# Optimization experiments

Measured on AMD Instinct MI355X. Metric: run time of the kernel, lower is better.

## Reference

```python
import jax, jax.numpy as jnp
import numpy as np

T, H, I, E, TOPK = 1024, 1024, 2048, 8, 2


def setup_inputs() -> dict:
    key = jax.random.key(0)
    k1, k2, k3, k4, k5, k6 = jax.random.split(key, 6)
    hidden_states = jax.random.normal(k1, (T, H), dtype=jnp.float32)
    expert_affinities = jax.random.uniform(k2, (T, E), dtype=jnp.float32)
    expert_index = jax.random.randint(k3, (T, TOPK), 0, E, dtype=jnp.int64)
    # Expert GLU MLP weights: gate/up [E,H,I], down [E,I,H]
    w_gate = jax.random.normal(k4, (E, H, I), dtype=jnp.float32) / np.sqrt(H)
    w_up = jax.random.normal(k5, (E, H, I), dtype=jnp.float32) / np.sqrt(H)
    w_down = jax.random.normal(k6, (E, I, H), dtype=jnp.float32) / np.sqrt(I)
    return {
        "hidden_states": hidden_states,
        "expert_affinities": expert_affinities,
        "expert_index": expert_index,
        "w_gate": w_gate,
        "w_up": w_up,
        "w_down": w_down,
        "seq_len": T,
    }


def reference(hidden_states, expert_affinities, expert_index, w_gate, w_up, w_down, seq_len):
    # Gather top-k affinities and renormalize (normalize_top_k_affinities=True)
    topk_aff = jnp.take_along_axis(expert_affinities, expert_index, axis=1)  # [T,K]
    topk_aff = topk_aff / jnp.sum(topk_aff, axis=1, keepdims=True)
    # Dense combine weights [T,E] (scatter of normalized top-k affinities)
    t_idx = jnp.arange(hidden_states.shape[0])[:, None]
    combine = jnp.zeros((hidden_states.shape[0], w_gate.shape[0]),
                        dtype=hidden_states.dtype).at[t_idx, expert_index].add(topk_aff)
    # GLU expert MLP for all experts (E small, grouped-GEMM form)
    g = jnp.einsum("th,ehi->tei", hidden_states, w_gate)  # [T,E,I]
    u = jnp.einsum("th,ehi->tei", hidden_states, w_up)    # [T,E,I]
    act = jax.nn.silu(g) * u                               # [T,E,I]
    # Down-projection fused with affinity-weighted combine
    out = jnp.einsum("tei,eih,te->th", act, w_down, combine)  # [T,H]
    return out
```

## Files before the change

kernel.cpp:

```cpp
#include <hip/hip_runtime.h>
#include <hip/hip_bf16.h>
#include <math.h>

#define T_ 1024
#define H_ 1024
#define I_ 2048
#define E_ 8
#define NSLOT 2048

#define BM 128
#define BN 64
#define BK 32
#define CHUNKS_PER_E (NSLOT / BM)
#define SPLITK2 2

typedef __attribute__((ext_vector_type(8))) short bf16x8;
typedef __attribute__((ext_vector_type(4))) float f32x4;
typedef __attribute__((ext_vector_type(4))) unsigned uint4v;

#define MFMA_BF16 __builtin_amdgcn_mfma_f32_16x16x32_bf16

__device__ __forceinline__ short f2bf(float f) {
  union { float f; unsigned u; } v; v.f = f;
  unsigned r = v.u + 0x7FFFu + ((v.u >> 16) & 1u);
  return (short)(r >> 16);
}
__device__ __forceinline__ unsigned cvtpk(float lo, float hi) {
  unsigned r;
  asm("v_cvt_pk_bf16_f32 %0, %1, %2" : "=v"(r) : "v"(lo), "v"(hi));
  return r;
}
__device__ __forceinline__ void gll16(const void* g, void* l) {
  __builtin_amdgcn_global_load_lds(
      (const __attribute__((address_space(1))) void*)g,
      (__attribute__((address_space(3))) void*)l, 16, 0, 0);
}

__device__ __forceinline__ void pipe_barrier() {
  __builtin_amdgcn_sched_barrier(0);
  asm volatile("s_waitcnt vmcnt(3) lgkmcnt(0)" ::: "memory");
  __builtin_amdgcn_s_barrier();
  __builtin_amdgcn_sched_barrier(0);
}
__device__ __forceinline__ void drain_barrier() {
  __builtin_amdgcn_sched_barrier(0);
  asm volatile("s_waitcnt vmcnt(0) lgkmcnt(0)" ::: "memory");
  __builtin_amdgcn_s_barrier();
  __builtin_amdgcn_sched_barrier(0);
}

__device__ __forceinline__ unsigned bswz(int n, int kbyte) {
  return (unsigned)(n * 64 + (kbyte ^ (((n >> 2) & 3) << 4)));
}

__global__ __launch_bounds__(256) void k_prep(const float* __restrict__ hs,
                                              short* __restrict__ hs_bf) {
  int i = (blockIdx.x * 256 + threadIdx.x) * 8;
  float4 v0 = *(const float4*)&hs[i];
  float4 v1 = *(const float4*)&hs[i + 4];
  uint4v p;
  p.x = cvtpk(v0.x, v0.y); p.y = cvtpk(v0.z, v0.w);
  p.z = cvtpk(v1.x, v1.y); p.w = cvtpk(v1.z, v1.w);
  *(uint4v*)&hs_bf[i] = p;
}

__global__ __launch_bounds__(1024) void k_build(
    const float* __restrict__ aff, const int* __restrict__ eidx,
    int* __restrict__ offs, int* __restrict__ slot_tok, float* __restrict__ slot_w) {
  __shared__ int cnt[E_];
  __shared__ int soff[E_ + 1];
  int t = threadIdx.x;
  if (t < E_) cnt[t] = 0;
  __syncthreads();
  int e0 = eidx[t * 2 + 0];
  int e1 = eidx[t * 2 + 1];
  float a0 = aff[t * E_ + e0];
  float a1 = aff[t * E_ + e1];
  float inv = 1.0f / (a0 + a1);
  int r0 = atomicAdd(&cnt[e0], 1);
  int r1 = atomicAdd(&cnt[e1], 1);
  __syncthreads();
  if (t == 0) {
    int s = 0;
    for (int e = 0; e < E_; ++e) { soff[e] = s; s += cnt[e]; }
    soff[E_] = s;
  }
  __syncthreads();
  if (t <= E_) offs[t] = soff[t];
  int s0 = soff[e0] + r0;
  int s1 = soff[e1] + r1;
  slot_tok[s0] = t; slot_w[s0] = a0 * inv;
  slot_tok[s1] = t; slot_w[s1] = a1 * inv;
}

__global__ __launch_bounds__(512, 4) void k_gemm1(
    const short* __restrict__ hs_bf, const float* __restrict__ wg,
    const float* __restrict__ wu, const int* __restrict__ offs,
    const int* __restrict__ slot_tok, short* __restrict__ act) {
  int e = blockIdx.y >> 4;
  int chunk = blockIdx.y & (CHUNKS_PER_E - 1);
  int lo = offs[e], hi = offs[e + 1];
  int row0 = lo + chunk * BM;
  if (row0 >= hi) return;
  int rows = min(BM, hi - row0);
  int i0 = blockIdx.x * BN;

  __shared__ short sA[4][BM * BK];
  __shared__ short sB[2][2][BN * BK];

  int tid = threadIdx.x;
  int lane = tid & 63;
  int w = tid >> 6;
  int wm = w >> 1, wn = w & 1;
  int lr = lane & 15;
  int lk = (lane >> 4) * 8;

  const float* wgE = wg + (size_t)e * H_ * I_;
  const float* wuE = wu + (size_t)e * H_ * I_;

  int ra = 16 * w + (lane >> 2);
  int tokA = slot_tok[row0 + min(ra, rows - 1)];
  const short* srcA = hs_bf + (size_t)tokA * H_ + (lane & 3) * 8;
  const float* wB = (w < 4) ? wgE : wuE;
  int mat = (w >= 4);
  int up = 4 * (w & 3) + (lane >> 4);
  int n4 = (lane & 15) * 4;
  const float* srcB = wB + (size_t)(2 * up) * I_ + i0 + n4;

  f32x4 accg[2][2], accu[2][2];
#pragma unroll
  for (int mr = 0; mr < 2; ++mr)
#pragma unroll
    for (int nr = 0; nr < 2; ++nr) {
      accg[mr][nr] = (f32x4){0.f, 0.f, 0.f, 0.f};
      accu[mr][nr] = (f32x4){0.f, 0.f, 0.f, 0.f};
    }

  float4 bs[2][2];

  gll16(srcA, &sA[0][w * 512]);
  bs[0][0] = *(const float4*)srcB;
  bs[0][1] = *(const float4*)(srcB + I_);
  gll16(srcA + BK, &sA[1][w * 512]);
  bs[1][0] = *(const float4*)(srcB + (size_t)BK * I_);
  bs[1][1] = *(const float4*)(srcB + (size_t)(BK + 1) * I_);
  {
    const float* p0 = (const float*)&bs[0][0];
    const float* p1 = (const float*)&bs[0][1];
#pragma unroll
    for (int j = 0; j < 4; ++j)
      *(unsigned*)((char*)&sB[0][mat][0] + bswz(n4 + j, 4 * up)) = cvtpk(p0[j], p1[j]);
  }
  drain_barrier();

  const int NT = H_ / BK;

#define G1_ITER(U, base_) do {                                                 \
    int t_ = (base_) + (U);                                                    \
    if (t_ + 2 < NT) {                                                         \
      int k2 = (t_ + 2) * BK;                                                  \
      gll16(srcA + k2, &sA[((U) + 2) & 3][w * 512]);                           \
      bs[(U) & 1][0] = *(const float4*)(srcB + (size_t)k2 * I_);               \
      bs[(U) & 1][1] = *(const float4*)(srcB + (size_t)(k2 + 1) * I_);         \
    }                                                                          \
    bf16x8 a0 = *(const bf16x8*)&sA[(U)][(wm * 32 + lr) * BK + lk];            \
    bf16x8 a1 = *(const bf16x8*)&sA[(U)][(wm * 32 + 16 + lr) * BK + lk];       \
    unsigned off0 = bswz(wn * 32 + lr, lk * 2);                                \
    unsigned off1 = bswz(wn * 32 + 16 + lr, lk * 2);                           \
    bf16x8 bg0 = *(const bf16x8*)((const char*)&sB[(U) & 1][0][0] + off0);     \
    bf16x8 bg1 = *(const bf16x8*)((const char*)&sB[(U) & 1][0][0] + off1);     \
    bf16x8 bu0 = *(const bf16x8*)((const char*)&sB[(U) & 1][1][0] + off0);     \
    bf16x8 bu1 = *(const bf16x8*)((const char*)&sB[(U) & 1][1][0] + off1);     \
    accg[0][0] = MFMA_BF16(a0, bg0, accg[0][0], 0, 0, 0);                      \
    accg[0][1] = MFMA_BF16(a0, bg1, accg[0][1], 0, 0, 0);                      \
    accg[1][0] = MFMA_BF16(a1, bg0, accg[1][0], 0, 0, 0);                      \
    accg[1][1] = MFMA_BF16(a1, bg1, accg[1][1], 0, 0, 0);                      \
    accu[0][0] = MFMA_BF16(a0, bu0, accu[0][0], 0, 0, 0);                      \
    accu[0][1] = MFMA_BF16(a0, bu1, accu[0][1], 0, 0, 0);                      \
    accu[1][0] = MFMA_BF16(a1, bu0, accu[1][0], 0, 0, 0);                      \
    accu[1][1] = MFMA_BF16(a1, bu1, accu[1][1], 0, 0, 0);                      \
    if (t_ + 1 < NT) {                                                         \
      const float* p0 = (const float*)&bs[((U) + 1) & 1][0];                   \
      const float* p1 = (const float*)&bs[((U) + 1) & 1][1];                   \
      _Pragma("unroll")                                                        \
      for (int j = 0; j < 4; ++j)                                              \
        *(unsigned*)((char*)&sB[((U) + 1) & 1][mat][0] + bswz(n4 + j, 4 * up)) \
            = cvtpk(p0[j], p1[j]);                                             \
    }                                                                          \
    pipe_barrier();                                                            \
  } while (0)

  for (int base = 0; base < NT; base += 4) {
    G1_ITER(0, base);
    G1_ITER(1, base);
    G1_ITER(2, base);
    G1_ITER(3, base);
  }
#undef G1_ITER

#pragma unroll
  for (int mr = 0; mr < 2; ++mr) {
#pragma unroll
    for (int r = 0; r < 4; ++r) {
      int m = wm * 32 + mr * 16 + (lane >> 4) * 4 + r;
      if (m < rows) {
#pragma unroll
        for (int nr = 0; nr < 2; ++nr) {
          float g = accg[mr][nr][r];
          float u = accu[mr][nr][r];
          float sg = 1.0f / (1.0f + __expf(-g));
          act[(size_t)(row0 + m) * I_ + i0 + wn * 32 + nr * 16 + lr] = f2bf(g * sg * u);
        }
      }
    }
  }
}

__global__ __launch_bounds__(512, 4) void k_gemm2(
    const short* __restrict__ act, const float* __restrict__ wd,
    const int* __restrict__ offs, const int* __restrict__ slot_tok,
    const float* __restrict__ slot_w, float* __restrict__ out) {
  int e = blockIdx.y >> 4;
  int chunk = blockIdx.y & (CHUNKS_PER_E - 1);
  int lo = offs[e], hi = offs[e + 1];
  int row0 = lo + chunk * BM;
  if (row0 >= hi) return;
  int rows = min(BM, hi - row0);
  int h0 = blockIdx.x * BN;
  int kbase = blockIdx.z * (I_ / SPLITK2);

  __shared__ short sA[4][BM * BK];
  __shared__ short sB[2][BN * BK];

  int tid = threadIdx.x;
  int lane = tid & 63;
  int w = tid >> 6;
  int wm = w >> 1, wn = w & 1;
  int lr = lane & 15;
  int lk = (lane >> 4) * 8;

  const float* wdE = wd + (size_t)e * I_ * H_;

  int ra = min(16 * w + (lane >> 2), rows - 1);
  const short* srcA = act + (size_t)(row0 + ra) * I_ + kbase + (lane & 3) * 8;
  int up = tid >> 5;
  int n2 = (tid & 31) * 2;
  const float* srcB = wdE + (size_t)(kbase + 2 * up) * H_ + h0 + n2;

  f32x4 acc[2][2];
#pragma unroll
  for (int mr = 0; mr < 2; ++mr)
#pragma unroll
    for (int nr = 0; nr < 2; ++nr)
      acc[mr][nr] = (f32x4){0.f, 0.f, 0.f, 0.f};

  float2 bs[2][2];

  gll16(srcA, &sA[0][w * 512]);
  bs[0][0] = *(const float2*)srcB;
  bs[0][1] = *(const float2*)(srcB + H_);
  gll16(srcA + BK, &sA[1][w * 512]);
  bs[1][0] = *(const float2*)(srcB + (size_t)BK * H_);
  bs[1][1] = *(const float2*)(srcB + (size_t)(BK + 1) * H_);
  *(unsigned*)((char*)&sB[0][0] + bswz(n2, 4 * up))     = cvtpk(bs[0][0].x, bs[0][1].x);
  *(unsigned*)((char*)&sB[0][0] + bswz(n2 + 1, 4 * up)) = cvtpk(bs[0][0].y, bs[0][1].y);
  drain_barrier();

  const int NT = (I_ / SPLITK2) / BK;

#define G2_ITER(U, base_) do {                                                 \
    int t_ = (base_) + (U);                                                    \
    if (t_ + 2 < NT) {                                                         \
      int k2 = (t_ + 2) * BK;                                                  \
      gll16(srcA + k2, &sA[((U) + 2) & 3][w * 512]);                           \
      bs[(U) & 1][0] = *(const float2*)(srcB + (size_t)k2 * H_);               \
      bs[(U) & 1][1] = *(const float2*)(srcB + (size_t)(k2 + 1) * H_);         \
    }                                                                          \
    bf16x8 a0 = *(const bf16x8*)&sA[(U)][(wm * 32 + lr) * BK + lk];            \
    bf16x8 a1 = *(const bf16x8*)&sA[(U)][(wm * 32 + 16 + lr) * BK + lk];       \
    bf16x8 b0 = *(const bf16x8*)((const char*)&sB[(U) & 1][0]                  \
                                 + bswz(wn * 32 + lr, lk * 2));                \
    bf16x8 b1 = *(const bf16x8*)((const char*)&sB[(U) & 1][0]                  \
                                 + bswz(wn * 32 + 16 + lr, lk * 2));           \
    acc[0][0] = MFMA_BF16(a0, b0, acc[0][0], 0, 0, 0);                         \
    acc[0][1] = MFMA_BF16(a0, b1, acc[0][1], 0, 0, 0);                         \
    acc[1][0] = MFMA_BF16(a1, b0, acc[1][0], 0, 0, 0);                         \
    acc[1][1] = MFMA_BF16(a1, b1, acc[1][1], 0, 0, 0);                         \
    if (t_ + 1 < NT) {                                                         \
      *(unsigned*)((char*)&sB[((U) + 1) & 1][0] + bswz(n2, 4 * up))            \
          = cvtpk(bs[((U) + 1) & 1][0].x, bs[((U) + 1) & 1][1].x);             \
      *(unsigned*)((char*)&sB[((U) + 1) & 1][0] + bswz(n2 + 1, 4 * up))        \
          = cvtpk(bs[((U) + 1) & 1][0].y, bs[((U) + 1) & 1][1].y);             \
    }                                                                          \
    pipe_barrier();                                                            \
  } while (0)

  for (int base = 0; base < NT; base += 4) {
    G2_ITER(0, base);
    G2_ITER(1, base);
    G2_ITER(2, base);
    G2_ITER(3, base);
  }
#undef G2_ITER

#pragma unroll
  for (int mr = 0; mr < 2; ++mr) {
#pragma unroll
    for (int r = 0; r < 4; ++r) {
      int m = wm * 32 + mr * 16 + (lane >> 4) * 4 + r;
      if (m < rows) {
        int gs = row0 + m;
        float wc = slot_w[gs];
        int tok = slot_tok[gs];
#pragma unroll
        for (int nr = 0; nr < 2; ++nr)
          atomicAdd(&out[(size_t)tok * H_ + h0 + wn * 32 + nr * 16 + lr],
                    acc[mr][nr][r] * wc);
      }
    }
  }
}

extern "C" void kernel_launch(void* const* d_in, const int* in_sizes, int n_in,
                              void* d_out, int out_size, void* d_ws, size_t ws_size,
                              hipStream_t stream) {
  const float* hs   = (const float*)d_in[0];
  const float* aff  = (const float*)d_in[1];
  const int*   eidx = (const int*)d_in[2];
  const float* wg   = (const float*)d_in[3];
  const float* wu   = (const float*)d_in[4];
  const float* wd   = (const float*)d_in[5];
  float* out = (float*)d_out;

  char* ws = (char*)d_ws;
  int*   offs     = (int*)ws;
  int*   slot_tok = (int*)(ws + 64);
  float* slot_w   = (float*)(ws + 64 + NSLOT * 4);
  short* hs_bf    = (short*)(ws + 64 + NSLOT * 8);
  short* act      = (short*)(ws + 64 + NSLOT * 8 + (size_t)T_ * H_ * 2);

  hipMemsetAsync(d_out, 0, (size_t)out_size * sizeof(float), stream);
  k_build<<<1, T_, 0, stream>>>(aff, eidx, offs, slot_tok, slot_w);
  k_prep<<<(T_ * H_) / (256 * 8), 256, 0, stream>>>(hs, hs_bf);
  k_gemm1<<<dim3(I_ / BN, E_ * CHUNKS_PER_E), 512, 0, stream>>>(hs_bf, wg, wu, offs, slot_tok, act);
  k_gemm2<<<dim3(H_ / BN, E_ * CHUNKS_PER_E, SPLITK2), 512, 0, stream>>>(act, wd, offs, slot_tok, slot_w, out);
}
```

Measured before the change: 105.5 us.

## Compact chunk list, narrow N tile, 4-wave blocks with swizzled A tiles

The routing kernel now emits a compact list of (expert, row-start) chunks, so both GEMM grids cover only real chunks (cap 24) instead of launching 16 mostly-empty chunk slots per expert. The N tile shrinks from 64 to 32 and blocks drop from 8 to 4 waves, each covering 32 rows with two A loads per step. An XOR swizzle is added to the A shared-memory tile to cut bank conflicts, and the wait counts are adjusted for the extra in-flight loads. This removes idle blocks and adds more blocks along N, at the cost of re-reading the A tile more often per output column. A NCHUNK_CAP of 24 assumes per-expert counts stay small enough; larger imbalance would silently drop chunks.

```diff
diff --git a/kernel.cpp b/kernel.cpp
--- a/kernel.cpp
+++ b/kernel.cpp
@@ -9,9 +9,9 @@
 #define NSLOT 2048
 
 #define BM 128
-#define BN 64
+#define BN 32
 #define BK 32
-#define CHUNKS_PER_E (NSLOT / BM)
+#define NCHUNK_CAP 24
 #define SPLITK2 2
 
 typedef __attribute__((ext_vector_type(8))) short bf16x8;
@@ -36,9 +36,15 @@
       (__attribute__((address_space(3))) void*)l, 16, 0, 0);
 }
 
-__device__ __forceinline__ void pipe_barrier() {
-  __builtin_amdgcn_sched_barrier(0);
-  asm volatile("s_waitcnt vmcnt(3) lgkmcnt(0)" ::: "memory");
+__device__ __forceinline__ void pipe_barrier6() {
+  __builtin_amdgcn_sched_barrier(0);
+  asm volatile("s_waitcnt vmcnt(6) lgkmcnt(0)" ::: "memory");
+  __builtin_amdgcn_s_barrier();
+  __builtin_amdgcn_sched_barrier(0);
+}
+__device__ __forceinline__ void pipe_barrier4() {
+  __builtin_amdgcn_sched_barrier(0);
+  asm volatile("s_waitcnt vmcnt(4) lgkmcnt(0)" ::: "memory");
   __builtin_amdgcn_s_barrier();
   __builtin_amdgcn_sched_barrier(0);
 }
@@ -51,6 +57,9 @@
 
 __device__ __forceinline__ unsigned bswz(int n, int kbyte) {
   return (unsigned)(n * 64 + (kbyte ^ (((n >> 2) & 3) << 4)));
+}
+__device__ __forceinline__ unsigned aswz(int r, int kbyte) {
+  return (unsigned)(r * 64 + (kbyte ^ (((r >> 1) & 3) << 4)));
 }
 
 __global__ __launch_bounds__(256) void k_prep(const float* __restrict__ hs,
@@ -66,7 +75,7 @@
 
 __global__ __launch_bounds__(1024) void k_build(
     const float* __restrict__ aff, const int* __restrict__ eidx,
-    int* __restrict__ offs, int* __restrict__ slot_tok, float* __restrict__ slot_w) {
+    int* __restrict__ meta, int* __restrict__ slot_tok, float* __restrict__ slot_w) {
   __shared__ int cnt[E_];
   __shared__ int soff[E_ + 1];
   int t = threadIdx.x;
@@ -84,25 +93,31 @@
     int s = 0;
     for (int e = 0; e < E_; ++e) { soff[e] = s; s += cnt[e]; }
     soff[E_] = s;
+    int nc = 0;
+    for (int e = 0; e < E_; ++e)
+      for (int c = soff[e]; c < soff[e] + cnt[e]; c += BM)
+        meta[16 + nc++] = e | (c << 8);
+    meta[9] = nc;
   }
   __syncthreads();
-  if (t <= E_) offs[t] = soff[t];
+  if (t <= E_) meta[t] = soff[t];
   int s0 = soff[e0] + r0;
   int s1 = soff[e1] + r1;
   slot_tok[s0] = t; slot_w[s0] = a0 * inv;
   slot_tok[s1] = t; slot_w[s1] = a1 * inv;
 }
 
-__global__ __launch_bounds__(512, 4) void k_gemm1(
+__global__ __launch_bounds__(256, 4) void k_gemm1(
     const short* __restrict__ hs_bf, const float* __restrict__ wg,
-    const float* __restrict__ wu, const int* __restrict__ offs,
+    const float* __restrict__ wu, const int* __restrict__ meta,
     const int* __restrict__ slot_tok, short* __restrict__ act) {
-  int e = blockIdx.y >> 4;
-  int chunk = blockIdx.y & (CHUNKS_PER_E - 1);
-  int lo = offs[e], hi = offs[e + 1];
-  int row0 = lo + chunk * BM;
-  if (row0 >= hi) return;
-  int rows = min(BM, hi - row0);
+  int nch = meta[9];
+  int yc = blockIdx.y;
+  if (yc >= nch) return;
+  int ck = meta[16 + yc];
+  int e = ck & 255;
+  int row0 = ck >> 8;
+  int rows = min(BM, meta[1 + e] - row0);
   int i0 = blockIdx.x * BN;
 
   __shared__ short sA[4][BM * BK];
@@ -111,21 +126,24 @@
   int tid = threadIdx.x;
   int lane = tid & 63;
   int w = tid >> 6;
-  int wm = w >> 1, wn = w & 1;
   int lr = lane & 15;
-  int lk = (lane >> 4) * 8;
+  int q = lane >> 4;
+  int lk = q * 8;
 
   const float* wgE = wg + (size_t)e * H_ * I_;
   const float* wuE = wu + (size_t)e * H_ * I_;
 
-  int ra = 16 * w + (lane >> 2);
-  int tokA = slot_tok[row0 + min(ra, rows - 1)];
-  const short* srcA = hs_bf + (size_t)tokA * H_ + (lane & 3) * 8;
-  const float* wB = (w < 4) ? wgE : wuE;
-  int mat = (w >= 4);
-  int up = 4 * (w & 3) + (lane >> 4);
-  int n4 = (lane & 15) * 4;
-  const float* srcB = wB + (size_t)(2 * up) * I_ + i0 + n4;
+  int r1 = 32 * w + (lane >> 2);
+  int kgel = ((lane & 3) ^ ((lane >> 3) & 3)) * 8;
+  int tok1 = slot_tok[row0 + min(r1, rows - 1)];
+  int tok2 = slot_tok[row0 + min(r1 + 16, rows - 1)];
+  const short* srcA1 = hs_bf + (size_t)tok1 * H_ + kgel;
+  const short* srcA2 = hs_bf + (size_t)tok2 * H_ + kgel;
+
+  int up = tid >> 4;
+  int n2 = (tid & 15) * 2;
+  const float* srcBg = wgE + (size_t)(2 * up) * I_ + i0 + n2;
+  const float* srcBu = wuE + (size_t)(2 * up) * I_ + i0 + n2;
 
   f32x4 accg[2][2], accu[2][2];
 #pragma unroll
@@ -136,21 +154,24 @@
       accu[mr][nr] = (f32x4){0.f, 0.f, 0.f, 0.f};
     }
 
-  float4 bs[2][2];
-
-  gll16(srcA, &sA[0][w * 512]);
-  bs[0][0] = *(const float4*)srcB;
-  bs[0][1] = *(const float4*)(srcB + I_);
-  gll16(srcA + BK, &sA[1][w * 512]);
-  bs[1][0] = *(const float4*)(srcB + (size_t)BK * I_);
-  bs[1][1] = *(const float4*)(srcB + (size_t)(BK + 1) * I_);
-  {
-    const float* p0 = (const float*)&bs[0][0];
-    const float* p1 = (const float*)&bs[0][1];
-#pragma unroll
-    for (int j = 0; j < 4; ++j)
-      *(unsigned*)((char*)&sB[0][mat][0] + bswz(n4 + j, 4 * up)) = cvtpk(p0[j], p1[j]);
-  }
+  float2 bg[2][2], bu[2][2];
+
+  gll16(srcA1, &sA[0][w * 1024]);
+  gll16(srcA2, &sA[0][w * 1024 + 512]);
+  bg[0][0] = *(const float2*)srcBg;
+  bg[0][1] = *(const float2*)(srcBg + I_);
+  bu[0][0] = *(const float2*)srcBu;
+  bu[0][1] = *(const float2*)(srcBu + I_);
+  gll16(srcA1 + BK, &sA[1][w * 1024]);
+  gll16(srcA2 + BK, &sA[1][w * 1024 + 512]);
+  bg[1][0] = *(const float2*)(srcBg + (size_t)BK * I_);
+  bg[1][1] = *(const float2*)(srcBg + (size_t)(BK + 1) * I_);
+  bu[1][0] = *(const float2*)(srcBu + (size_t)BK * I_);
+  bu[1][1] = *(const float2*)(srcBu + (size_t)(BK + 1) * I_);
+  *(unsigned*)((char*)&sB[0][0][0] + bswz(n2, 4 * up))     = cvtpk(bg[0][0].x, bg[0][1].x);
+  *(unsigned*)((char*)&sB[0][0][0] + bswz(n2 + 1, 4 * up)) = cvtpk(bg[0][0].y, bg[0][1].y);
+  *(unsigned*)((char*)&sB[0][1][0] + bswz(n2, 4 * up))     = cvtpk(bu[0][0].x, bu[0][1].x);
+  *(unsigned*)((char*)&sB[0][1][0] + bswz(n2 + 1, 4 * up)) = cvtpk(bu[0][0].y, bu[0][1].y);
   drain_barrier();
 
   const int NT = H_ / BK;
@@ -159,35 +180,43 @@
     int t_ = (base_) + (U);                                                    \
     if (t_ + 2 < NT) {                                                         \
       int k2 = (t_ + 2) * BK;                                                  \
-      gll16(srcA + k2, &sA[((U) + 2) & 3][w * 512]);                           \
-      bs[(U) & 1][0] = *(const float4*)(srcB + (size_t)k2 * I_);               \
-      bs[(U) & 1][1] = *(const float4*)(srcB + (size_t)(k2 + 1) * I_);         \
+      gll16(srcA1 + k2, &sA[((U) + 2) & 3][w * 1024]);                         \
+      gll16(srcA2 + k2, &sA[((U) + 2) & 3][w * 1024 + 512]);                   \
+      bg[(U) & 1][0] = *(const float2*)(srcBg + (size_t)k2 * I_);              \
+      bg[(U) & 1][1] = *(const float2*)(srcBg + (size_t)(k2 + 1) * I_);        \
+      bu[(U) & 1][0] = *(const float2*)(srcBu + (size_t)k2 * I_);              \
+      bu[(U) & 1][1] = *(const float2*)(srcBu + (size_t)(k2 + 1) * I_);        \
     }                                                                          \
-    bf16x8 a0 = *(const bf16x8*)&sA[(U)][(wm * 32 + lr) * BK + lk];            \
-    bf16x8 a1 = *(const bf16x8*)&sA[(U)][(wm * 32 + 16 + lr) * BK + lk];       \
-    unsigned off0 = bswz(wn * 32 + lr, lk * 2);                                \
-    unsigned off1 = bswz(wn * 32 + 16 + lr, lk * 2);                           \
-    bf16x8 bg0 = *(const bf16x8*)((const char*)&sB[(U) & 1][0][0] + off0);     \
-    bf16x8 bg1 = *(const bf16x8*)((const char*)&sB[(U) & 1][0][0] + off1);     \
-    bf16x8 bu0 = *(const bf16x8*)((const char*)&sB[(U) & 1][1][0] + off0);     \
-    bf16x8 bu1 = *(const bf16x8*)((const char*)&sB[(U) & 1][1][0] + off1);     \
-    accg[0][0] = MFMA_BF16(a0, bg0, accg[0][0], 0, 0, 0);                      \
-    accg[0][1] = MFMA_BF16(a0, bg1, accg[0][1], 0, 0, 0);                      \
-    accg[1][0] = MFMA_BF16(a1, bg0, accg[1][0], 0, 0, 0);                      \
-    accg[1][1] = MFMA_BF16(a1, bg1, accg[1][1], 0, 0, 0);                      \
-    accu[0][0] = MFMA_BF16(a0, bu0, accu[0][0], 0, 0, 0);                      \
-    accu[0][1] = MFMA_BF16(a0, bu1, accu[0][1], 0, 0, 0);                      \
-    accu[1][0] = MFMA_BF16(a1, bu0, accu[1][0], 0, 0, 0);                      \
-    accu[1][1] = MFMA_BF16(a1, bu1, accu[1][1], 0, 0, 0);                      \
+    bf16x8 a0 = *(const bf16x8*)((const char*)&sA[(U)][0]                      \
+                                 + aswz(w * 32 + lr, lk * 2));                 \
+    bf16x8 a1 = *(const bf16x8*)((const char*)&sA[(U)][0]                      \
+                                 + aswz(w * 32 + 16 + lr, lk * 2));            \
+    unsigned off0 = bswz(lr, lk * 2);                                          \
+    unsigned off1 = bswz(16 + lr, lk * 2);                                     \
+    bf16x8 fg0 = *(const bf16x8*)((const char*)&sB[(U) & 1][0][0] + off0);     \
+    bf16x8 fg1 = *(const bf16x8*)((const char*)&sB[(U) & 1][0][0] + off1);     \
+    bf16x8 fu0 = *(const bf16x8*)((const char*)&sB[(U) & 1][1][0] + off0);     \
+    bf16x8 fu1 = *(const bf16x8*)((const char*)&sB[(U) & 1][1][0] + off1);     \
+    accg[0][0] = MFMA_BF16(a0, fg0, accg[0][0], 0, 0, 0);                      \
+    accg[0][1] = MFMA_BF16(a0, fg1, accg[0][1], 0, 0, 0);                      \
+    accg[1][0] = MFMA_BF16(a1, fg0, accg[1][0], 0, 0, 0);                      \
+    accg[1][1] = MFMA_BF16(a1, fg1, accg[1][1], 0, 0, 0);                      \
+    accu[0][0] = MFMA_BF16(a0, fu0, accu[0][0], 0, 0, 0);                      \
+    accu[0][1] = MFMA_BF16(a0, fu1, accu[0][1], 0, 0, 0);                      \
+    accu[1][0] = MFMA_BF16(a1, fu0, accu[1][0], 0, 0, 0);                      \
+    accu[1][1] = MFMA_BF16(a1, fu1, accu[1][1], 0, 0, 0);                      \
     if (t_ + 1 < NT) {                                                         \
-      const float* p0 = (const float*)&bs[((U) + 1) & 1][0];                   \
-      const float* p1 = (const float*)&bs[((U) + 1) & 1][1];                   \
-      _Pragma("unroll")                                                        \
-      for (int j = 0; j < 4; ++j)                                              \
-        *(unsigned*)((char*)&sB[((U) + 1) & 1][mat][0] + bswz(n4 + j, 4 * up)) \
-            = cvtpk(p0[j], p1[j]);                                             \
+      int s_ = ((U) + 1) & 1;                                                  \
+      *(unsigned*)((char*)&sB[s_][0][0] + bswz(n2, 4 * up))                    \
+          = cvtpk(bg[s_][0].x, bg[s_][1].x);                                   \
+      *(unsigned*)((char*)&sB[s_][0][0] + bswz(n2 + 1, 4 * up))                \
+          = cvtpk(bg[s_][0].y, bg[s_][1].y);                                   \
+      *(unsigned*)((char*)&sB[s_][1][0] + bswz(n2, 4 * up))                    \
+          = cvtpk(bu[s_][0].x, bu[s_][1].x);                                   \
+      *(unsigned*)((char*)&sB[s_][1][0] + bswz(n2 + 1, 4 * up))                \
+          = cvtpk(bu[s_][0].y, bu[s_][1].y);                                   \
     }                                                                          \
-    pipe_barrier();                                                            \
+    pipe_barrier6();                                                           \
   } while (0)
 
   for (int base = 0; base < NT; base += 4) {
@@ -202,30 +231,31 @@
   for (int mr = 0; mr < 2; ++mr) {
 #pragma unroll
     for (int r = 0; r < 4; ++r) {
-      int m = wm * 32 + mr * 16 + (lane >> 4) * 4 + r;
+      int m = w * 32 + mr * 16 + q * 4 + r;
       if (m < rows) {
 #pragma unroll
         for (int nr = 0; nr < 2; ++nr) {
           float g = accg[mr][nr][r];
           float u = accu[mr][nr][r];
           float sg = 1.0f / (1.0f + __expf(-g));
-          act[(size_t)(row0 + m) * I_ + i0 + wn * 32 + nr * 16 + lr] = f2bf(g * sg * u);
+          act[(size_t)(row0 + m) * I_ + i0 + nr * 16 + lr] = f2bf(g * sg * u);
         }
       }
     }
   }
 }
 
-__global__ __launch_bounds__(512, 4) void k_gemm2(
+__global__ __launch_bounds__(256, 4) void k_gemm2(
     const short* __restrict__ act, const float* __restrict__ wd,
-    const int* __restrict__ offs, const int* __restrict__ slot_tok,
+    const int* __restrict__ meta, const int* __restrict__ slot_tok,
     const float* __restrict__ slot_w, float* __restrict__ out) {
-  int e = blockIdx.y >> 4;
-  int chunk = blockIdx.y & (CHUNKS_PER_E - 1);
-  int lo = offs[e], hi = offs[e + 1];
-  int row0 = lo + chunk * BM;
-  if (row0 >= hi) return;
-  int rows = min(BM, hi - row0);
+  int nch = meta[9];
+  int yc = blockIdx.y;
+  if (yc >= nch) return;
+  int ck = meta[16 + yc];
+  int e = ck & 255;
+  int row0 = ck >> 8;
+  int rows = min(BM, meta[1 + e] - row0);
   int h0 = blockIdx.x * BN;
   int kbase = blockIdx.z * (I_ / SPLITK2);
 
@@ -235,16 +265,19 @@
   int tid = threadIdx.x;
   int lane = tid & 63;
   int w = tid >> 6;
-  int wm = w >> 1, wn = w & 1;
   int lr = lane & 15;
-  int lk = (lane >> 4) * 8;
+  int q = lane >> 4;
+  int lk = q * 8;
 
   const float* wdE = wd + (size_t)e * I_ * H_;
 
-  int ra = min(16 * w + (lane >> 2), rows - 1);
-  const short* srcA = act + (size_t)(row0 + ra) * I_ + kbase + (lane & 3) * 8;
-  int up = tid >> 5;
-  int n2 = (tid & 31) * 2;
+  int r1 = 32 * w + (lane >> 2);
+  int kgel = ((lane & 3) ^ ((lane >> 3) & 3)) * 8;
+  const short* srcA1 = act + (size_t)(row0 + min(r1, rows - 1)) * I_ + kbase + kgel;
+  const short* srcA2 = act + (size_t)(row0 + min(r1 + 16, rows - 1)) * I_ + kbase + kgel;
+
+  int up = tid >> 4;
+  int n2 = (tid & 15) * 2;
   const float* srcB = wdE + (size_t)(kbase + 2 * up) * H_ + h0 + n2;
 
   f32x4 acc[2][2];
@@ -254,16 +287,18 @@
     for (int nr = 0; nr < 2; ++nr)
       acc[mr][nr] = (f32x4){0.f, 0.f, 0.f, 0.f};
 
-  float2 bs[2][2];
-
-  gll16(srcA, &sA[0][w * 512]);
-  bs[0][0] = *(const float2*)srcB;
-  bs[0][1] = *(const float2*)(srcB + H_);
-  gll16(srcA + BK, &sA[1][w * 512]);
-  bs[1][0] = *(const float2*)(srcB + (size_t)BK * H_);
-  bs[1][1] = *(const float2*)(srcB + (size_t)(BK + 1) * H_);
-  *(unsigned*)((char*)&sB[0][0] + bswz(n2, 4 * up))     = cvtpk(bs[0][0].x, bs[0][1].x);
-  *(unsigned*)((char*)&sB[0][0] + bswz(n2 + 1, 4 * up)) = cvtpk(bs[0][0].y, bs[0][1].y);
+  float2 bd[2][2];
+
+  gll16(srcA1, &sA[0][w * 1024]);
+  gll16(srcA2, &sA[0][w * 1024 + 512]);
+  bd[0][0] = *(const float2*)srcB;
+  bd[0][1] = *(const float2*)(srcB + H_);
+  gll16(srcA1 + BK, &sA[1][w * 1024]);
+  gll16(srcA2 + BK, &sA[1][w * 1024 + 512]);
+  bd[1][0] = *(const float2*)(srcB + (size_t)BK * H_);
+  bd[1][1] = *(const float2*)(srcB + (size_t)(BK + 1) * H_);
+  *(unsigned*)((char*)&sB[0][0] + bswz(n2, 4 * up))     = cvtpk(bd[0][0].x, bd[0][1].x);
+  *(unsigned*)((char*)&sB[0][0] + bswz(n2 + 1, 4 * up)) = cvtpk(bd[0][0].y, bd[0][1].y);
   drain_barrier();
 
   const int NT = (I_ / SPLITK2) / BK;
@@ -272,27 +307,31 @@
     int t_ = (base_) + (U);                                                    \
     if (t_ + 2 < NT) {                                                         \
       int k2 = (t_ + 2) * BK;                                                  \
-      gll16(srcA + k2, &sA[((U) + 2) & 3][w * 512]);                           \
-      bs[(U) & 1][0] = *(const float2*)(srcB + (size_t)k2 * H_);               \
-      bs[(U) & 1][1] = *(const float2*)(srcB + (size_t)(k2 + 1) * H_);         \
+      gll16(srcA1 + k2, &sA[((U) + 2) & 3][w * 1024]);                         \
+      gll16(srcA2 + k2, &sA[((U) + 2) & 3][w * 1024 + 512]);                   \
+      bd[(U) & 1][0] = *(const float2*)(srcB + (size_t)k2 * H_);               \
+      bd[(U) & 1][1] = *(const float2*)(srcB + (size_t)(k2 + 1) * H_);         \
     }                                                                          \
-    bf16x8 a0 = *(const bf16x8*)&sA[(U)][(wm * 32 + lr) * BK + lk];            \
-    bf16x8 a1 = *(const bf16x8*)&sA[(U)][(wm * 32 + 16 + lr) * BK + lk];       \
+    bf16x8 a0 = *(const bf16x8*)((const char*)&sA[(U)][0]                      \
+                                 + aswz(w * 32 + lr, lk * 2));                 \
+    bf16x8 a1 = *(const bf16x8*)((const char*)&sA[(U)][0]                      \
+                                 + aswz(w * 32 + 16 + lr, lk * 2));            \
     bf16x8 b0 = *(const bf16x8*)((const char*)&sB[(U) & 1][0]                  \
-                                 + bswz(wn * 32 + lr, lk * 2));                \
+                                 + bswz(lr, lk * 2));                          \
     bf16x8 b1 = *(const bf16x8*)((const char*)&sB[(U) & 1][0]                  \
-                                 + bswz(wn * 32 + 16 + lr, lk * 2));           \
+                                 + bswz(16 + lr, lk * 2));                     \
     acc[0][0] = MFMA_BF16(a0, b0, acc[0][0], 0, 0, 0);                         \
     acc[0][1] = MFMA_BF16(a0, b1, acc[0][1], 0, 0, 0);                         \
     acc[1][0] = MFMA_BF16(a1, b0, acc[1][0], 0, 0, 0);                         \
     acc[1][1] = MFMA_BF16(a1, b1, acc[1][1], 0, 0, 0);                         \
     if (t_ + 1 < NT) {                                                         \
-      *(unsigned*)((char*)&sB[((U) + 1) & 1][0] + bswz(n2, 4 * up))            \
-          = cvtpk(bs[((U) + 1) & 1][0].x, bs[((U) + 1) & 1][1].x);             \
-      *(unsigned*)((char*)&sB[((U) + 1) & 1][0] + bswz(n2 + 1, 4 * up))        \
-          = cvtpk(bs[((U) + 1) & 1][0].y, bs[((U) + 1) & 1][1].y);             \
+      int s_ = ((U) + 1) & 1;                                                  \
+      *(unsigned*)((char*)&sB[s_][0] + bswz(n2, 4 * up))                       \
+          = cvtpk(bd[s_][0].x, bd[s_][1].x);                                   \
+      *(unsigned*)((char*)&sB[s_][0] + bswz(n2 + 1, 4 * up))                   \
+          = cvtpk(bd[s_][0].y, bd[s_][1].y);                                   \
     }                                                                          \
-    pipe_barrier();                                                            \
+    pipe_barrier4();                                                           \
   } while (0)
 
   for (int base = 0; base < NT; base += 4) {
@@ -307,14 +346,14 @@
   for (int mr = 0; mr < 2; ++mr) {
 #pragma unroll
     for (int r = 0; r < 4; ++r) {
-      int m = wm * 32 + mr * 16 + (lane >> 4) * 4 + r;
+      int m = w * 32 + mr * 16 + q * 4 + r;
       if (m < rows) {
         int gs = row0 + m;
         float wc = slot_w[gs];
         int tok = slot_tok[gs];
 #pragma unroll
         for (int nr = 0; nr < 2; ++nr)
-          atomicAdd(&out[(size_t)tok * H_ + h0 + wn * 32 + nr * 16 + lr],
+          atomicAdd(&out[(size_t)tok * H_ + h0 + nr * 16 + lr],
                     acc[mr][nr][r] * wc);
       }
     }
@@ -333,15 +372,15 @@
   float* out = (float*)d_out;
 
   char* ws = (char*)d_ws;
-  int*   offs     = (int*)ws;
-  int*   slot_tok = (int*)(ws + 64);
-  float* slot_w   = (float*)(ws + 64 + NSLOT * 4);
-  short* hs_bf    = (short*)(ws + 64 + NSLOT * 8);
-  short* act      = (short*)(ws + 64 + NSLOT * 8 + (size_t)T_ * H_ * 2);
+  int*   meta     = (int*)ws;
+  int*   slot_tok = (int*)(ws + 256);
+  float* slot_w   = (float*)(ws + 256 + NSLOT * 4);
+  short* hs_bf    = (short*)(ws + 256 + NSLOT * 8);
+  short* act      = (short*)(ws + 256 + NSLOT * 8 + (size_t)T_ * H_ * 2);
 
   hipMemsetAsync(d_out, 0, (size_t)out_size * sizeof(float), stream);
-  k_build<<<1, T_, 0, stream>>>(aff, eidx, offs, slot_tok, slot_w);
+  k_build<<<1, T_, 0, stream>>>(aff, eidx, meta, slot_tok, slot_w);
   k_prep<<<(T_ * H_) / (256 * 8), 256, 0, stream>>>(hs, hs_bf);
-  k_gemm1<<<dim3(I_ / BN, E_ * CHUNKS_PER_E), 512, 0, stream>>>(hs_bf, wg, wu, offs, slot_tok, act);
-  k_gemm2<<<dim3(H_ / BN, E_ * CHUNKS_PER_E, SPLITK2), 512, 0, stream>>>(act, wd, offs, slot_tok, slot_w, out);
-}
+  k_gemm1<<<dim3(I_ / BN, NCHUNK_CAP), 256, 0, stream>>>(hs_bf, wg, wu, meta, slot_tok, act);
+  k_gemm2<<<dim3(H_ / BN, NCHUNK_CAP, SPLITK2), 256, 0, stream>>>(act, wd, meta, slot_tok, slot_w, out);
+}
```

New measurement: 122.4 us. 1.16x slower.

## Compact the expert chunk list and deepen the GEMM prefetch pipeline to three stages

Applied to the files above, without the earlier changes.

The routing kernel now builds a compact list of (expert, row-start) chunks. Both GEMMs launch only a capped number of y-blocks and index into that list, instead of launching 16 chunks per expert where most blocks exit immediately. The load pipeline in both GEMMs also prefetches three K-tiles ahead, using a 4-deep register ring for the B operand and relaxing the vmcnt wait to 6, so more memory latency can be hidden. The cost is higher register pressure from the larger B staging buffers, and a fixed chunk cap of 24 that has to bound the worst-case chunk count.

```diff
diff --git a/kernel.cpp b/kernel.cpp
--- a/kernel.cpp
+++ b/kernel.cpp
@@ -11,7 +11,7 @@
 #define BM 128
 #define BN 64
 #define BK 32
-#define CHUNKS_PER_E (NSLOT / BM)
+#define NCHUNK_CAP 24
 #define SPLITK2 2
 
 typedef __attribute__((ext_vector_type(8))) short bf16x8;
@@ -36,9 +36,9 @@
       (__attribute__((address_space(3))) void*)l, 16, 0, 0);
 }
 
-__device__ __forceinline__ void pipe_barrier() {
+__device__ __forceinline__ void pipe_barrier6() {
   __builtin_amdgcn_sched_barrier(0);
-  asm volatile("s_waitcnt vmcnt(3) lgkmcnt(0)" ::: "memory");
+  asm volatile("s_waitcnt vmcnt(6) lgkmcnt(0)" ::: "memory");
   __builtin_amdgcn_s_barrier();
   __builtin_amdgcn_sched_barrier(0);
 }
@@ -66,7 +66,7 @@
 
 __global__ __launch_bounds__(1024) void k_build(
     const float* __restrict__ aff, const int* __restrict__ eidx,
-    int* __restrict__ offs, int* __restrict__ slot_tok, float* __restrict__ slot_w) {
+    int* __restrict__ meta, int* __restrict__ slot_tok, float* __restrict__ slot_w) {
   __shared__ int cnt[E_];
   __shared__ int soff[E_ + 1];
   int t = threadIdx.x;
@@ -84,9 +84,14 @@
     int s = 0;
     for (int e = 0; e < E_; ++e) { soff[e] = s; s += cnt[e]; }
     soff[E_] = s;
+    int nc = 0;
+    for (int e = 0; e < E_; ++e)
+      for (int c = soff[e]; c < soff[e] + cnt[e]; c += BM)
+        meta[16 + nc++] = e | (c << 8);
+    meta[9] = nc;
   }
   __syncthreads();
-  if (t <= E_) offs[t] = soff[t];
+  if (t <= E_) meta[t] = soff[t];
   int s0 = soff[e0] + r0;
   int s1 = soff[e1] + r1;
   slot_tok[s0] = t; slot_w[s0] = a0 * inv;
@@ -95,14 +100,15 @@
 
 __global__ __launch_bounds__(512, 4) void k_gemm1(
     const short* __restrict__ hs_bf, const float* __restrict__ wg,
-    const float* __restrict__ wu, const int* __restrict__ offs,
+    const float* __restrict__ wu, const int* __restrict__ meta,
     const int* __restrict__ slot_tok, short* __restrict__ act) {
-  int e = blockIdx.y >> 4;
-  int chunk = blockIdx.y & (CHUNKS_PER_E - 1);
-  int lo = offs[e], hi = offs[e + 1];
-  int row0 = lo + chunk * BM;
-  if (row0 >= hi) return;
-  int rows = min(BM, hi - row0);
+  int nch = meta[9];
+  int yc = blockIdx.y;
+  if (yc >= nch) return;
+  int ck = meta[16 + yc];
+  int e = ck & 255;
+  int row0 = ck >> 8;
+  int rows = min(BM, meta[1 + e] - row0);
   int i0 = blockIdx.x * BN;
 
   __shared__ short sA[4][BM * BK];
@@ -136,14 +142,14 @@
       accu[mr][nr] = (f32x4){0.f, 0.f, 0.f, 0.f};
     }
 
-  float4 bs[2][2];
-
-  gll16(srcA, &sA[0][w * 512]);
-  bs[0][0] = *(const float4*)srcB;
-  bs[0][1] = *(const float4*)(srcB + I_);
-  gll16(srcA + BK, &sA[1][w * 512]);
-  bs[1][0] = *(const float4*)(srcB + (size_t)BK * I_);
-  bs[1][1] = *(const float4*)(srcB + (size_t)(BK + 1) * I_);
+  float4 bs[4][2];
+
+#pragma unroll
+  for (int p = 0; p < 3; ++p) {
+    gll16(srcA + p * BK, &sA[p][w * 512]);
+    bs[p][0] = *(const float4*)(srcB + (size_t)(p * BK) * I_);
+    bs[p][1] = *(const float4*)(srcB + (size_t)(p * BK + 1) * I_);
+  }
   {
     const float* p0 = (const float*)&bs[0][0];
     const float* p1 = (const float*)&bs[0][1];
@@ -157,11 +163,11 @@
 
 #define G1_ITER(U, base_) do {                                                 \
     int t_ = (base_) + (U);                                                    \
-    if (t_ + 2 < NT) {                                                         \
-      int k2 = (t_ + 2) * BK;                                                  \
-      gll16(srcA + k2, &sA[((U) + 2) & 3][w * 512]);                           \
-      bs[(U) & 1][0] = *(const float4*)(srcB + (size_t)k2 * I_);               \
-      bs[(U) & 1][1] = *(const float4*)(srcB + (size_t)(k2 + 1) * I_);         \
+    if (t_ + 3 < NT) {                                                         \
+      int k3 = (t_ + 3) * BK;                                                  \
+      gll16(srcA + k3, &sA[((U) + 3) & 3][w * 512]);                           \
+      bs[((U) + 3) & 3][0] = *(const float4*)(srcB + (size_t)k3 * I_);         \
+      bs[((U) + 3) & 3][1] = *(const float4*)(srcB + (size_t)(k3 + 1) * I_);   \
     }                                                                          \
     bf16x8 a0 = *(const bf16x8*)&sA[(U)][(wm * 32 + lr) * BK + lk];            \
     bf16x8 a1 = *(const bf16x8*)&sA[(U)][(wm * 32 + 16 + lr) * BK + lk];       \
@@ -180,14 +186,14 @@
     accu[1][0] = MFMA_BF16(a1, bu0, accu[1][0], 0, 0, 0);                      \
     accu[1][1] = MFMA_BF16(a1, bu1, accu[1][1], 0, 0, 0);                      \
     if (t_ + 1 < NT) {                                                         \
-      const float* p0 = (const float*)&bs[((U) + 1) & 1][0];                   \
-      const float* p1 = (const float*)&bs[((U) + 1) & 1][1];                   \
+      const float* p0 = (const float*)&bs[((U) + 1) & 3][0];                   \
+      const float* p1 = (const float*)&bs[((U) + 1) & 3][1];                   \
       _Pragma("unroll")                                                        \
       for (int j = 0; j < 4; ++j)                                              \
         *(unsigned*)((char*)&sB[((U) + 1) & 1][mat][0] + bswz(n4 + j, 4 * up)) \
             = cvtpk(p0[j], p1[j]);                                             \
     }                                                                          \
-    pipe_barrier();                                                            \
+    pipe_barrier6();                                                           \
   } while (0)
 
   for (int base = 0; base < NT; base += 4) {
@@ -218,14 +224,15 @@
 
 __global__ __launch_bounds__(512, 4) void k_gemm2(
     const short* __restrict__ act, const float* __restrict__ wd,
-    const int* __restrict__ offs, const int* __restrict__ slot_tok,
+    const int* __restrict__ meta, const int* __restrict__ slot_tok,
     const float* __restrict__ slot_w, float* __restrict__ out) {
-  int e = blockIdx.y >> 4;
-  int chunk = blockIdx.y & (CHUNKS_PER_E - 1);
-  int lo = offs[e], hi = offs[e + 1];
-  int row0 = lo + chunk * BM;
-  if (row0 >= hi) return;
-  int rows = min(BM, hi - row0);
+  int nch = meta[9];
+  int yc = blockIdx.y;
+  if (yc >= nch) return;
+  int ck = meta[16 + yc];
+  int e = ck & 255;
+  int row0 = ck >> 8;
+  int rows = min(BM, meta[1 + e] - row0);
   int h0 = blockIdx.x * BN;
   int kbase = blockIdx.z * (I_ / SPLITK2);
 
@@ -254,14 +261,14 @@
     for (int nr = 0; nr < 2; ++nr)
       acc[mr][nr] = (f32x4){0.f, 0.f, 0.f, 0.f};
 
-  float2 bs[2][2];
-
-  gll16(srcA, &sA[0][w * 512]);
-  bs[0][0] = *(const float2*)srcB;
-  bs[0][1] = *(const float2*)(srcB + H_);
-  gll16(srcA + BK, &sA[1][w * 512]);
-  bs[1][0] = *(const float2*)(srcB + (size_t)BK * H_);
-  bs[1][1] = *(const float2*)(srcB + (size_t)(BK + 1) * H_);
+  float2 bs[4][2];
+
+#pragma unroll
+  for (int p = 0; p < 3; ++p) {
+    gll16(srcA + p * BK, &sA[p][w * 512]);
+    bs[p][0] = *(const float2*)(srcB + (size_t)(p * BK) * H_);
+    bs[p][1] = *(const float2*)(srcB + (size_t)(p * BK + 1) * H_);
+  }
   *(unsigned*)((char*)&sB[0][0] + bswz(n2, 4 * up))     = cvtpk(bs[0][0].x, bs[0][1].x);
   *(unsigned*)((char*)&sB[0][0] + bswz(n2 + 1, 4 * up)) = cvtpk(bs[0][0].y, bs[0][1].y);
   drain_barrier();
@@ -270,11 +277,11 @@
 
 #define G2_ITER(U, base_) do {                                                 \
     int t_ = (base_) + (U);                                                    \
-    if (t_ + 2 < NT) {                                                         \
-      int k2 = (t_ + 2) * BK;                                                  \
-      gll16(srcA + k2, &sA[((U) + 2) & 3][w * 512]);                           \
-      bs[(U) & 1][0] = *(const float2*)(srcB + (size_t)k2 * H_);               \
-      bs[(U) & 1][1] = *(const float2*)(srcB + (size_t)(k2 + 1) * H_);         \
+    if (t_ + 3 < NT) {                                                         \
+      int k3 = (t_ + 3) * BK;                                                  \
+      gll16(srcA + k3, &sA[((U) + 3) & 3][w * 512]);                           \
+      bs[((U) + 3) & 3][0] = *(const float2*)(srcB + (size_t)k3 * H_);         \
+      bs[((U) + 3) & 3][1] = *(const float2*)(srcB + (size_t)(k3 + 1) * H_);   \
     }                                                                          \
     bf16x8 a0 = *(const bf16x8*)&sA[(U)][(wm * 32 + lr) * BK + lk];            \
     bf16x8 a1 = *(const bf16x8*)&sA[(U)][(wm * 32 + 16 + lr) * BK + lk];       \
@@ -287,12 +294,13 @@
     acc[1][0] = MFMA_BF16(a1, b0, acc[1][0], 0, 0, 0);                         \
     acc[1][1] = MFMA_BF16(a1, b1, acc[1][1], 0, 0, 0);                         \
     if (t_ + 1 < NT) {                                                         \
+      int s_ = ((U) + 1) & 3;                                                  \
       *(unsigned*)((char*)&sB[((U) + 1) & 1][0] + bswz(n2, 4 * up))            \
-          = cvtpk(bs[((U) + 1) & 1][0].x, bs[((U) + 1) & 1][1].x);             \
+          = cvtpk(bs[s_][0].x, bs[s_][1].x);                                   \
       *(unsigned*)((char*)&sB[((U) + 1) & 1][0] + bswz(n2 + 1, 4 * up))        \
-          = cvtpk(bs[((U) + 1) & 1][0].y, bs[((U) + 1) & 1][1].y);             \
+          = cvtpk(bs[s_][0].y, bs[s_][1].y);                                   \
     }                                                                          \
-    pipe_barrier();                                                            \
+    pipe_barrier6();                                                           \
   } while (0)
 
   for (int base = 0; base < NT; base += 4) {
@@ -333,15 +341,15 @@
   float* out = (float*)d_out;
 
   char* ws = (char*)d_ws;
-  int*   offs     = (int*)ws;
-  int*   slot_tok = (int*)(ws + 64);
-  float* slot_w   = (float*)(ws + 64 + NSLOT * 4);
-  short* hs_bf    = (short*)(ws + 64 + NSLOT * 8);
-  short* act      = (short*)(ws + 64 + NSLOT * 8 + (size_t)T_ * H_ * 2);
+  int*   meta     = (int*)ws;
+  int*   slot_tok = (int*)(ws + 256);
+  float* slot_w   = (float*)(ws + 256 + NSLOT * 4);
+  short* hs_bf    = (short*)(ws + 256 + NSLOT * 8);
+  short* act      = (short*)(ws + 256 + NSLOT * 8 + (size_t)T_ * H_ * 2);
 
   hipMemsetAsync(d_out, 0, (size_t)out_size * sizeof(float), stream);
-  k_build<<<1, T_, 0, stream>>>(aff, eidx, offs, slot_tok, slot_w);
+  k_build<<<1, T_, 0, stream>>>(aff, eidx, meta, slot_tok, slot_w);
   k_prep<<<(T_ * H_) / (256 * 8), 256, 0, stream>>>(hs, hs_bf);
-  k_gemm1<<<dim3(I_ / BN, E_ * CHUNKS_PER_E), 512, 0, stream>>>(hs_bf, wg, wu, offs, slot_tok, act);
-  k_gemm2<<<dim3(H_ / BN, E_ * CHUNKS_PER_E, SPLITK2), 512, 0, stream>>>(act, wd, offs, slot_tok, slot_w, out);
-}
+  k_gemm1<<<dim3(I_ / BN, NCHUNK_CAP), 512, 0, stream>>>(hs_bf, wg, wu, meta, slot_tok, act);
+  k_gemm2<<<dim3(H_ / BN, NCHUNK_CAP, SPLITK2), 512, 0, stream>>>(act, wd, meta, slot_tok, slot_w, out);
+}
```

After: 102.2 us. 1.03x faster.
